# Kernel optimization log

Hardware: AMD Instinct MI355X
Metric: run time of the kernel (lower is better)

Reference implementation:

```python
import jax, jax.numpy as jnp
import numpy as np

B, S, D_MODEL, N_HEADS, D_FF = 4, 2048, 1024, 16, 4096
HEAD_DIM = D_MODEL // N_HEADS
NUM_BUCKETS, MAX_DISTANCE = 32, 128
EPS = 1e-6


def _relative_position_bucket(relative_position, num_buckets=NUM_BUCKETS, max_distance=MAX_DISTANCE):
    # bidirectional (encoder) variant, matching T5RelativePositionBias
    n = -relative_position
    nb = num_buckets // 2
    ret = (n < 0).astype(jnp.int32) * nb
    n = jnp.abs(n)
    max_exact = nb // 2
    val_if_large = max_exact + (
        jnp.log(jnp.maximum(n, 1).astype(jnp.float32) / max_exact)
        / np.log(max_distance / max_exact) * (nb - max_exact)
    ).astype(jnp.int32)
    val_if_large = jnp.minimum(val_if_large, nb - 1)
    return ret + jnp.where(n < max_exact, n, val_if_large)


def t5_position_bias(rel_emb, q_len, k_len):
    ctx = jnp.arange(q_len)[:, None]
    mem = jnp.arange(k_len)[None, :]
    rp_bucket = _relative_position_bucket(mem - ctx)          # [S, S]
    bias = rel_emb[rp_bucket]                                  # [S, S, H]
    return jnp.transpose(bias, (2, 0, 1))[None]                # [1, H, S, S]


def layer_norm(x, g, b):
    mu = jnp.mean(x, axis=-1, keepdims=True)
    var = jnp.mean(jnp.square(x - mu), axis=-1, keepdims=True)
    return (x - mu) * jax.lax.rsqrt(var + EPS) * g + b


def setup_inputs() -> dict:
    key = jax.random.key(0)
    ks = jax.random.split(key, 20)
    s = 0.02
    p = {
        'src': jax.random.normal(ks[0], (B, S, D_MODEL), jnp.float32),
        'wq': jax.random.normal(ks[1], (D_MODEL, D_MODEL), jnp.float32) * s,
        'bq': jnp.zeros((D_MODEL,), jnp.float32),
        'wk': jax.random.normal(ks[2], (D_MODEL, D_MODEL), jnp.float32) * s,
        'bk': jnp.zeros((D_MODEL,), jnp.float32),
        'wv': jax.random.normal(ks[3], (D_MODEL, D_MODEL), jnp.float32) * s,
        'bv': jnp.zeros((D_MODEL,), jnp.float32),
        'wo': jax.random.normal(ks[4], (D_MODEL, D_MODEL), jnp.float32) * s,
        'bo': jnp.zeros((D_MODEL,), jnp.float32),
        'w1': jax.random.normal(ks[5], (D_MODEL, D_FF), jnp.float32) * s,
        'b1': jnp.zeros((D_FF,), jnp.float32),
        'w2': jax.random.normal(ks[6], (D_FF, D_MODEL), jnp.float32) * s,
        'b2': jnp.zeros((D_MODEL,), jnp.float32),
        'ln1_g': jnp.ones((D_MODEL,), jnp.float32),
        'ln1_b': jnp.zeros((D_MODEL,), jnp.float32),
        'ln2_g': jnp.ones((D_MODEL,), jnp.float32),
        'ln2_b': jnp.zeros((D_MODEL,), jnp.float32),
        'rel_emb': jax.random.normal(ks[7], (NUM_BUCKETS, N_HEADS), jnp.float32) * s,
    }
    return p


def reference(src, wq, bq, wk, bk, wv, bv, wo, bo, w1, b1, w2, b2,
              ln1_g, ln1_b, ln2_g, ln2_b, rel_emb):
    b, s, _ = src.shape

    # --- self-attention block (pre-norm) ---
    xn = layer_norm(src, ln1_g, ln1_b)
    q = (xn @ wq + bq).reshape(b, s, N_HEADS, HEAD_DIM).transpose(0, 2, 1, 3)
    k = (xn @ wk + bk).reshape(b, s, N_HEADS, HEAD_DIM).transpose(0, 2, 1, 3)
    v = (xn @ wv + bv).reshape(b, s, N_HEADS, HEAD_DIM).transpose(0, 2, 1, 3)

    bias = t5_position_bias(rel_emb, s, s)                       # [1,H,S,S]
    scores = jnp.einsum('bhqd,bhkd->bhqk', q, k) / np.sqrt(HEAD_DIM) + bias
    attn = jax.nn.softmax(scores, axis=-1)
    ctx = jnp.einsum('bhqk,bhkd->bhqd', attn, v)                 # [B,H,S,Dh]
    ctx = ctx.transpose(0, 2, 1, 3).reshape(b, s, D_MODEL)
    x = src + (ctx @ wo + bo)

    # --- FFN block (pre-norm, ReLU) ---
    yn = layer_norm(x, ln2_g, ln2_b)
    y = jax.nn.relu(yn @ w1 + b1) @ w2 + b2
    return x + y
```

## Files before the change

kernel.cpp:

```cpp
#include <hip/hip_runtime.h>
#include <math.h>

typedef unsigned short u16;

#define S_LEN 2048
#define BSZ 4
#define DM 1024
#define NH 16
#define HD 64
#define DFF 4096
#define ROWS (BSZ * S_LEN)
#define LOG2E 1.4426950408889634f

typedef __attribute__((__ext_vector_type__(8))) __bf16 bf16x8;
typedef __attribute__((__ext_vector_type__(8))) short short8;
typedef __attribute__((__ext_vector_type__(4))) short short4v;
typedef __attribute__((__ext_vector_type__(4))) float f32x4;
typedef __attribute__((__ext_vector_type__(4))) float float4v;

__device__ __forceinline__ float bf2f(u16 u) {
    union { unsigned int i; float f; } c; c.i = ((unsigned int)u) << 16; return c.f;
}
__device__ __forceinline__ u16 f2bf(float f) {
    union { float f; unsigned int i; } c; c.f = f;
    unsigned int r = c.i + 0x7fffu + ((c.i >> 16) & 1u);
    return (u16)(r >> 16);
}
__device__ __forceinline__ u16 f2bf_cvt(float f) {
    __bf16 h = (__bf16)f;
    return __builtin_bit_cast(u16, h);
}
__device__ __forceinline__ float ldin(const void* p, long i, int f32) {
    return f32 ? ((const float*)p)[i] : bf2f(((const u16*)p)[i]);
}
__device__ __forceinline__ int dtype_f32(const u16* ln1g) {
    return ln1g[0] != 0x3F80;
}
__device__ __forceinline__ void gl_lds16(const void* g, void* l) {
    __builtin_amdgcn_global_load_lds(
        (const __attribute__((address_space(1))) unsigned int*)g,
        (__attribute__((address_space(3))) unsigned int*)l, 16, 0, 0);
}

__device__ __forceinline__ void tr_tile(
    const void* __restrict__ src, u16* __restrict__ dst, int N, int K,
    int bx, int by, int f32, int tid, u16 (*t)[72])
{
#pragma unroll
    for (int i = 0; i < 2; i++) {
        int c = tid + i * 256;
        int row = c >> 3, col = (c & 7) * 8;
        long off = (long)(by * 64 + row) * N + bx * 64 + col;
        short8 v;
        if (f32) {
            const float* s = (const float*)src + off;
            float4v a = *(const float4v*)s;
            float4v b = *(const float4v*)(s + 4);
#pragma unroll
            for (int k = 0; k < 4; k++) { v[k] = (short)f2bf(a[k]); v[k + 4] = (short)f2bf(b[k]); }
        } else {
            v = *(const short8*)((const u16*)src + off);
        }
        *(short8*)(&t[row][col]) = v;
    }
    __syncthreads();
#pragma unroll
    for (int i = 0; i < 2; i++) {
        int c = tid + i * 256;
        int row = c >> 3, col = (c & 7) * 8;
        short8 v;
#pragma unroll
        for (int jj = 0; jj < 8; jj++) v[jj] = (short)t[col + jj][row];
        *(short8*)(dst + (long)(bx * 64 + row) * K + by * 64 + col) = v;
    }
}

__global__ __launch_bounds__(256) void transpose4(
    const void* wq, const void* wk, const void* wv, const void* wo,
    u16* __restrict__ wqkvt, u16* __restrict__ wot, const u16* __restrict__ ln1g)
{
    __shared__ u16 t[64][72];
    int z = blockIdx.z;
    const void* src = (z == 0) ? wq : (z == 1) ? wk : (z == 2) ? wv : wo;
    u16* dst = (z < 3) ? wqkvt + (long)z * 1024 * 1024 : wot;
    tr_tile(src, dst, DM, DM, blockIdx.x, blockIdx.y, dtype_f32(ln1g), threadIdx.x, t);
}

__global__ __launch_bounds__(256) void transpose2(
    const void* w1, const void* w2, u16* __restrict__ w1t, u16* __restrict__ w2t,
    const u16* __restrict__ ln1g)
{
    __shared__ u16 t[64][72];
    int f32 = dtype_f32(ln1g);
    if (blockIdx.z == 0)
        tr_tile(w1, w1t, DFF, DM, blockIdx.x, blockIdx.y, f32, threadIdx.x, t);
    else
        tr_tile(w2, w2t, DM, DFF, blockIdx.y, blockIdx.x, f32, threadIdx.x, t);
}

__global__ __launch_bounds__(256) void vtrans(
    const u16* __restrict__ v, u16* __restrict__ vt)
{
    __shared__ u16 t[64][72];
    int s0 = blockIdx.x * 64;
    int bh = blockIdx.y;
    const u16* src = v + (long)bh * S_LEN * HD;
    u16* dst = vt + (long)bh * HD * S_LEN;
    int tid = threadIdx.x;
#pragma unroll
    for (int i = 0; i < 2; i++) {
        int c = tid + i * 256;
        int row = c >> 3, col = (c & 7) * 8;
        *(short8*)(&t[row][col]) = *(const short8*)(src + (long)(s0 + row) * HD + col);
    }
    __syncthreads();
#pragma unroll
    for (int i = 0; i < 2; i++) {
        int c = tid + i * 256;
        int row = c >> 3, col = (c & 7) * 8;
        short8 o;
#pragma unroll
        for (int jj = 0; jj < 8; jj++) o[jj] = (short)t[col + jj][row];
        *(short8*)(dst + (long)row * S_LEN + s0 + col) = o;
    }
}

__global__ __launch_bounds__(256) void prep_kernel(
    const void* bq, const void* bk, const void* bv, const void* bo,
    const void* b1, const void* b2, const void* l1g, const void* l1b,
    const void* l2g, const void* l2b, const void* rel,
    u16* __restrict__ smalls, float* __restrict__ bias_full)
{
    int f32 = dtype_f32((const u16*)l1g);
    int tid = blockIdx.x * blockDim.x + threadIdx.x;
    if (tid < 13312) {
        float v;
        if      (tid < 1024)  v = ldin(bq,  tid,         f32);
        else if (tid < 2048)  v = ldin(bk,  tid - 1024,  f32);
        else if (tid < 3072)  v = ldin(bv,  tid - 2048,  f32);
        else if (tid < 4096)  v = ldin(bo,  tid - 3072,  f32);
        else if (tid < 8192)  v = ldin(b1,  tid - 4096,  f32);
        else if (tid < 9216)  v = ldin(b2,  tid - 8192,  f32);
        else if (tid < 10240) v = ldin(l1g, tid - 9216,  f32);
        else if (tid < 11264) v = ldin(l1b, tid - 10240, f32);
        else if (tid < 12288) v = ldin(l2g, tid - 11264, f32);
        else                  v = ldin(l2b, tid - 12288, f32);
        smalls[tid] = f2bf(v);
    }
    if (tid < 4095 * 16) {
        int dIdx = tid >> 4;
        int h = tid & 15;
        int delta = dIdx - 2047;
        int n = -delta;
        int ret = (n < 0) ? 16 : 0;
        int na = (n < 0) ? -n : n;
        int bkt;
        if (na < 8) {
            bkt = na;
        } else {
            float tval = logf((float)na * 0.125f) * 2.8853900817779268f;
            int v = 8 + (int)tval;
            bkt = v < 15 ? v : 15;
        }
        bkt += ret;
        bias_full[h * 4095 + dIdx] = ldin(rel, bkt * 16 + h, f32) * LOG2E;
    }
}

__global__ __launch_bounds__(256) void ln_kernel(
    const void* __restrict__ xin, int external, const u16* __restrict__ ln1g,
    const u16* __restrict__ g, const u16* __restrict__ bta, u16* __restrict__ out)
{
    int f32 = external ? dtype_f32(ln1g) : 0;
    int row = blockIdx.x;
    int tid = threadIdx.x;
    float vals[4];
    if (f32) {
        float4v v = *(const float4v*)((const float*)xin + (long)row * DM + tid * 4);
#pragma unroll
        for (int k = 0; k < 4; k++) vals[k] = v[k];
    } else {
        short4v v = *(const short4v*)((const u16*)xin + (long)row * DM + tid * 4);
#pragma unroll
        for (int k = 0; k < 4; k++) vals[k] = bf2f((u16)v[k]);
    }
    float s1 = 0.f, s2 = 0.f;
#pragma unroll
    for (int k = 0; k < 4; k++) { s1 += vals[k]; s2 += vals[k] * vals[k]; }
#pragma unroll
    for (int off = 32; off > 0; off >>= 1) {
        s1 += __shfl_xor(s1, off);
        s2 += __shfl_xor(s2, off);
    }
    __shared__ float ps1[4], ps2[4];
    int wave = tid >> 6, lane = tid & 63;
    if (lane == 0) { ps1[wave] = s1; ps2[wave] = s2; }
    __syncthreads();
    s1 = ps1[0] + ps1[1] + ps1[2] + ps1[3];
    s2 = ps2[0] + ps2[1] + ps2[2] + ps2[3];
    float mu = s1 * (1.0f / DM);
    float var = s2 * (1.0f / DM) - mu * mu;
    float rs = rsqrtf(var + 1e-6f);
    short4v ov;
#pragma unroll
    for (int k = 0; k < 4; k++) {
        float gv = bf2f(g[tid * 4 + k]);
        float bv = bf2f(bta[tid * 4 + k]);
        ov[k] = (short)f2bf((vals[k] - mu) * rs * gv + bv);
    }
    *(short4v*)(out + (long)row * DM + tid * 4) = ov;
}

#define BM 128
#define BN 128
#define BK 64

__global__ __launch_bounds__(256, 3) void gemm_bt(
    const u16* __restrict__ A, const u16* __restrict__ Bt,
    const u16* __restrict__ bias, int M, int N, int K, int mode,
    u16* __restrict__ out_q, u16* __restrict__ out_k, u16* __restrict__ out_v,
    const void* __restrict__ res, void* __restrict__ outp,
    const u16* __restrict__ ln1g)
{
    __shared__ u16 As[BM][BK];
    __shared__ u16 Bs[BN][BK];
    int tid = threadIdx.x;
    int wave = tid >> 6, lane = tid & 63;
    int quad = lane >> 4, l16 = lane & 15;
    int wr = (wave >> 1) * 64, wc = (wave & 1) * 64;

    int nwg = gridDim.x * gridDim.y;
    int bid = blockIdx.y * gridDim.x + blockIdx.x;
    int chunk = nwg >> 3;
    int swz = (bid & 7) * chunk + (bid >> 3);
    int bx = swz % gridDim.x, by = swz / gridDim.x;

    long m0 = (long)by * BM, n0 = (long)bx * BN;
    int flg = (mode == 2 || mode == 4) ? dtype_f32(ln1g) : 0;

    int prow = tid >> 3;
    int pchk = tid & 7;
    int cchk = pchk ^ (prow & 7);
    int skc = cchk * 8;
    int pkc = pchk * 8;
    int rxor = l16 & 7;

    f32x4 acc[4][4];
    f32x4 z = {0.f, 0.f, 0.f, 0.f};
#pragma unroll
    for (int i = 0; i < 4; i++)
#pragma unroll
        for (int j = 0; j < 4; j++) acc[i][j] = z;

    for (int k0 = 0; k0 < K; k0 += BK) {
        __syncthreads();
#pragma unroll
        for (int ro = 0; ro < 4; ro++) {
            gl_lds16(A  + (m0 + ro * 32 + prow) * K + k0 + skc, &As[ro * 32 + prow][pkc]);
            gl_lds16(Bt + (n0 + ro * 32 + prow) * K + k0 + skc, &Bs[ro * 32 + prow][pkc]);
        }
        __syncthreads();
#pragma unroll
        for (int t = 0; t < 2; t++) {
            int rc = ((t * 4 + quad) ^ rxor) * 8;
            bf16x8 af[4], bfr[4];
#pragma unroll
            for (int i = 0; i < 4; i++)
                af[i] = __builtin_bit_cast(bf16x8, *(const short8*)(&As[wr + i * 16 + l16][rc]));
#pragma unroll
            for (int j = 0; j < 4; j++)
                bfr[j] = __builtin_bit_cast(bf16x8, *(const short8*)(&Bs[wc + j * 16 + l16][rc]));
#pragma unroll
            for (int i = 0; i < 4; i++)
#pragma unroll
                for (int j = 0; j < 4; j++)
                    acc[i][j] = __builtin_amdgcn_mfma_f32_16x16x32_bf16(af[i], bfr[j], acc[i][j], 0, 0, 0);
        }
    }

#pragma unroll
    for (int i = 0; i < 4; i++) {
#pragma unroll
        for (int j = 0; j < 4; j++) {
#pragma unroll
            for (int r = 0; r < 4; r++) {
                long gr = m0 + wr + i * 16 + quad * 4 + r;
                long gc = n0 + wc + j * 16 + l16;
                float val = acc[i][j][r] + bf2f(bias[gc]);
                if (mode == 1) {
                    int sel = (int)(gc >> 10);
                    int cc = (int)(gc & 1023);
                    int h = cc >> 6, d = cc & 63;
                    int b = (int)(gr >> 11), s = (int)(gr & 2047);
                    u16* dst = (sel == 0) ? out_q : (sel == 1 ? out_k : out_v);
                    dst[(((long)(b * NH + h)) * S_LEN + s) * HD + d] = f2bf(val);
                } else if (mode == 2) {
                    long idx = gr * N + gc;
                    float rv = flg ? ((const float*)res)[idx]
                                   : bf2f(((const u16*)res)[idx]);
                    ((u16*)outp)[idx] = f2bf(val + rv);
                } else if (mode == 3) {
                    ((u16*)outp)[gr * N + gc] = f2bf(val > 0.f ? val : 0.f);
                } else {
                    long idx = gr * N + gc;
                    float o = val + bf2f(((const u16*)res)[idx]);
                    if (flg) ((float*)outp)[idx] = o;
                    else     ((u16*)outp)[idx]  = f2bf(o);
                }
            }
        }
    }
}

__global__ __launch_bounds__(256, 4) void attn_kernel(
    const u16* __restrict__ Qg, const u16* __restrict__ Kg, const u16* __restrict__ Vtg,
    const float* __restrict__ bias_full, u16* __restrict__ ctx)
{
    __shared__ u16 Ks[64][64];
    __shared__ u16 Vt[64][64];
    __shared__ u16 Ps[64][72];
    __shared__ u16 bias_s[2112];

    int bh = blockIdx.y;
    int b = bh >> 4, h = bh & 15;
    int q0 = blockIdx.x * 64;
    const u16* Q  = Qg  + (long)bh * S_LEN * HD;
    const u16* Kp = Kg  + (long)bh * S_LEN * HD;
    const u16* Vp = Vtg + (long)bh * HD * S_LEN;

    int tid = threadIdx.x;
    int wave = tid >> 6, lane = tid & 63;
    int quad = lane >> 4, l16 = lane & 15;

    for (int i = tid; i < 2112; i += 256)
        bias_s[i] = f2bf(bias_full[h * 4095 + 1984 + i - q0]);
    float Bneg = bias_full[h * 4095 + 0];
    float Bpos = bias_full[h * 4095 + 4094];

    int prow = tid >> 3, pchk = tid & 7;
    int cchk = pchk ^ (prow & 7);
    int rxor = l16 & 7;
    int rc0 = (quad ^ rxor) * 8;
    int rc1 = ((4 + quad) ^ rxor) * 8;

    bf16x8 aq[2];
#pragma unroll
    for (int t = 0; t < 2; t++)
        aq[t] = __builtin_bit_cast(bf16x8,
            *(const short8*)(Q + (long)(q0 + wave * 16 + l16) * HD + t * 32 + quad * 8));

    bf16x8 ones;
#pragma unroll
    for (int i = 0; i < 8; i++) ones[i] = (__bf16)1.0f;

    f32x4 o[4];
    f32x4 z = {0.f, 0.f, 0.f, 0.f};
#pragma unroll
    for (int j = 0; j < 4; j++) o[j] = z;
    f32x4 lacc = z;

    int ib = 63 + quad * 4 - wave * 16 - l16;
    const float c0 = 0.125f * LOG2E;

    for (int t0 = 0; t0 < S_LEN; t0 += 64) {
        __syncthreads();
#pragma unroll
        for (int ro = 0; ro < 2; ro++) {
            gl_lds16(Kp + (long)(t0 + ro * 32 + prow) * HD + cchk * 8,
                     &Ks[ro * 32 + prow][pchk * 8]);
            gl_lds16(Vp + (long)(ro * 32 + prow) * S_LEN + t0 + cchk * 8,
                     &Vt[ro * 32 + prow][pchk * 8]);
        }
        __syncthreads();

        f32x4 s_[4];
#pragma unroll
        for (int j = 0; j < 4; j++) {
            f32x4 a = z;
            bf16x8 kf0 = __builtin_bit_cast(bf16x8, *(const short8*)(&Ks[j * 16 + l16][rc0]));
            a = __builtin_amdgcn_mfma_f32_16x16x32_bf16(kf0, aq[0], a, 0, 0, 0);
            bf16x8 kf1 = __builtin_bit_cast(bf16x8, *(const short8*)(&Ks[j * 16 + l16][rc1]));
            a = __builtin_amdgcn_mfma_f32_16x16x32_bf16(kf1, aq[1], a, 0, 0, 0);
            s_[j] = a;
        }
        int d0 = t0 - q0;
        int nearb = (d0 >= -153 && d0 <= 153);
        float bconst = (d0 > 0) ? Bpos : Bneg;
#pragma unroll
        for (int j = 0; j < 4; j++) {
            short4v pk;
#pragma unroll
            for (int r = 0; r < 4; r++) {
                float bl = nearb ? bf2f(bias_s[ib + t0 + j * 16 + r]) : bconst;
                float p = __builtin_amdgcn_exp2f(fminf(fmaf(s_[j][r], c0, bl), 100.0f));
                pk[r] = (short)f2bf_cvt(p);
            }
            *(short4v*)(&Ps[wave * 16 + l16][j * 16 + quad * 4]) = pk;
        }

        bf16x8 ap[2];
#pragma unroll
        for (int tt = 0; tt < 2; tt++)
            ap[tt] = __builtin_bit_cast(bf16x8,
                *(const short8*)(&Ps[wave * 16 + l16][tt * 32 + quad * 8]));
        lacc = __builtin_amdgcn_mfma_f32_16x16x32_bf16(ap[0], ones, lacc, 0, 0, 0);
        lacc = __builtin_amdgcn_mfma_f32_16x16x32_bf16(ap[1], ones, lacc, 0, 0, 0);
#pragma unroll
        for (int j = 0; j < 4; j++) {
            f32x4 t = o[j];
            bf16x8 bv0 = __builtin_bit_cast(bf16x8, *(const short8*)(&Vt[j * 16 + l16][rc0]));
            t = __builtin_amdgcn_mfma_f32_16x16x32_bf16(ap[0], bv0, t, 0, 0, 0);
            bf16x8 bv1 = __builtin_bit_cast(bf16x8, *(const short8*)(&Vt[j * 16 + l16][rc1]));
            t = __builtin_amdgcn_mfma_f32_16x16x32_bf16(ap[1], bv1, t, 0, 0, 0);
            o[j] = t;
        }
    }

#pragma unroll
    for (int r = 0; r < 4; r++) {
        int qr = wave * 16 + quad * 4 + r;
        float linv = 1.0f / lacc[r];
        long srow = (long)(b * S_LEN + q0 + qr);
#pragma unroll
        for (int j = 0; j < 4; j++)
            ctx[srow * DM + h * HD + j * 16 + l16] = f2bf(o[j][r] * linv);
    }
}

extern "C" void kernel_launch(void* const* d_in, const int* in_sizes, int n_in,
                              void* d_out, int out_size, void* d_ws, size_t ws_size,
                              hipStream_t stream)
{
    const void* src  = d_in[0];
    const void* wq   = d_in[1];
    const void* bq   = d_in[2];
    const void* wk   = d_in[3];
    const void* bk   = d_in[4];
    const void* wv   = d_in[5];
    const void* bv   = d_in[6];
    const void* wo   = d_in[7];
    const void* bo   = d_in[8];
    const void* w1   = d_in[9];
    const void* b1   = d_in[10];
    const void* w2   = d_in[11];
    const void* b2   = d_in[12];
    const void* ln1g = d_in[13];
    const void* ln1b = d_in[14];
    const void* ln2g = d_in[15];
    const void* ln2b = d_in[16];
    const void* rel  = d_in[17];
    const u16* l1g16 = (const u16*)ln1g;

    char* ws = (char*)d_ws;
    const long MB = 1L << 20;
    u16*   smalls = (u16*)  (ws);
    float* bfull  = (float*)(ws + 65536);
    u16*   xn     = (u16*)  (ws + 1  * MB);
    u16*   vtg    = (u16*)  (ws + 1  * MB);
    u16*   qws    = (u16*)  (ws + 17 * MB);
    u16*   kws    = (u16*)  (ws + 33 * MB);
    u16*   vws    = (u16*)  (ws + 49 * MB);
    u16*   hbuf   = (u16*)  (ws + 1  * MB);
    u16*   ctx    = (u16*)  (ws + 65 * MB);
    u16*   yn     = (u16*)  (ws + 65 * MB);
    u16*   xbf    = (u16*)  (ws + 81 * MB);
    u16*   wqkvt  = (u16*)  (ws + 97 * MB);
    u16*   wot    = (u16*)  (ws + 103 * MB);
    u16*   w1t    = (u16*)  (ws + 97 * MB);
    u16*   w2t    = (u16*)  (ws + 105 * MB);

    transpose4<<<dim3(16, 16, 4), 256, 0, stream>>>(wq, wk, wv, wo, wqkvt, wot, l1g16);
    prep_kernel<<<256, 256, 0, stream>>>(bq, bk, bv, bo, b1, b2,
                                         ln1g, ln1b, ln2g, ln2b, rel,
                                         smalls, bfull);

    ln_kernel<<<ROWS, 256, 0, stream>>>(src, 1, l1g16,
                                        smalls + 9216, smalls + 10240, xn);

    gemm_bt<<<dim3(3072 / BN, ROWS / BM), 256, 0, stream>>>(
        xn, wqkvt, smalls + 0, ROWS, 3072, DM, 1,
        qws, kws, vws, nullptr, nullptr, l1g16);

    vtrans<<<dim3(S_LEN / 64, BSZ * NH), 256, 0, stream>>>(vws, vtg);

    attn_kernel<<<dim3(S_LEN / 64, BSZ * NH), 256, 0, stream>>>(qws, kws, vtg, bfull, ctx);

    gemm_bt<<<dim3(DM / BN, ROWS / BM), 256, 0, stream>>>(
        ctx, wot, smalls + 3072, ROWS, DM, DM, 2,
        nullptr, nullptr, nullptr, src, xbf, l1g16);

    transpose2<<<dim3(64, 16, 2), 256, 0, stream>>>(w1, w2, w1t, w2t, l1g16);

    ln_kernel<<<ROWS, 256, 0, stream>>>(xbf, 0, l1g16,
                                        smalls + 11264, smalls + 12288, yn);

    gemm_bt<<<dim3(DFF / BN, ROWS / BM), 256, 0, stream>>>(
        yn, w1t, smalls + 4096, ROWS, DFF, DM, 3,
        nullptr, nullptr, nullptr, nullptr, hbuf, l1g16);

    gemm_bt<<<dim3(DM / BN, ROWS / BM), 256, 0, stream>>>(
        hbuf, w2t, smalls + 8192, ROWS, DM, DFF, 4,
        nullptr, nullptr, nullptr, xbf, d_out, l1g16);
}
```

Measured before the change: 597.4 us.

## Add 256x256 pipelined GEMM kernel for QKV and FFN1 projections

Introduces a new 512-thread GEMM with 256x256 output tiles, double-buffered LDS fed by direct global-to-LDS loads, XOR-swizzled LDS layout, and a hand-scheduled phase pipeline using explicit waitcnt/barrier and setprio. Workgroup IDs are remapped so neighbouring blocks share operands in cache. The QKV and FFN-up projections switch to this kernel to raise arithmetic intensity per LDS load and overlap memory with MFMA. The larger tiles produce fewer workgroups (e.g. 384 for QKV), which may underfill the GPU, and the manual vmcnt accounting is fragile.

```diff
diff --git a/kernel.cpp b/kernel.cpp
--- a/kernel.cpp
+++ b/kernel.cpp
@@ -41,6 +41,11 @@
         (const __attribute__((address_space(1))) unsigned int*)g,
         (__attribute__((address_space(3))) unsigned int*)l, 16, 0, 0);
 }
+
+#define BARR  asm volatile("s_barrier" ::: "memory")
+#define LGKM0 asm volatile("s_waitcnt lgkmcnt(0)" ::: "memory")
+#define VM4   asm volatile("s_waitcnt vmcnt(4)" ::: "memory")
+#define VM0   asm volatile("s_waitcnt vmcnt(0)" ::: "memory")
 
 __device__ __forceinline__ void tr_tile(
     const void* __restrict__ src, u16* __restrict__ dst, int N, int K,
@@ -312,6 +317,145 @@
     }
 }
 
+#define TM 256
+#define TN 256
+#define TK 64
+
+#define PHASE(bi, q, STAGE, WAITV)                                             \
+    {                                                                          \
+        if ((q) == 0) {                                                        \
+            _Pragma("unroll")                                                  \
+            for (int j = 0; j < 4; j++) {                                      \
+                _Pragma("unroll")                                              \
+                for (int t = 0; t < 2; t++)                                    \
+                    bfr[j][t] = __builtin_bit_cast(bf16x8, *(const short8*)(   \
+                        &Bs[bi][wn * 64 + j * 16 + l16][((t * 4 + quad) ^ rxor) * 8])); \
+            }                                                                  \
+        }                                                                      \
+        _Pragma("unroll")                                                      \
+        for (int i = 0; i < 2; i++) {                                          \
+            _Pragma("unroll")                                                  \
+            for (int t = 0; t < 2; t++)                                        \
+                af[i][t] = __builtin_bit_cast(bf16x8, *(const short8*)(        \
+                    &As[bi][wm * 128 + ((q) * 2 + i) * 16 + l16][((t * 4 + quad) ^ rxor) * 8])); \
+        }                                                                      \
+        STAGE                                                                  \
+        WAITV;                                                                 \
+        BARR;                                                                  \
+        LGKM0;                                                                 \
+        __builtin_amdgcn_sched_barrier(0);                                     \
+        __builtin_amdgcn_s_setprio(1);                                         \
+        _Pragma("unroll")                                                      \
+        for (int i = 0; i < 2; i++) {                                          \
+            _Pragma("unroll")                                                  \
+            for (int j = 0; j < 4; j++) {                                      \
+                acc[(q) * 2 + i][j] = __builtin_amdgcn_mfma_f32_16x16x32_bf16( \
+                    af[i][0], bfr[j][0], acc[(q) * 2 + i][j], 0, 0, 0);        \
+                acc[(q) * 2 + i][j] = __builtin_amdgcn_mfma_f32_16x16x32_bf16( \
+                    af[i][1], bfr[j][1], acc[(q) * 2 + i][j], 0, 0, 0);        \
+            }                                                                  \
+        }                                                                      \
+        __builtin_amdgcn_s_setprio(0);                                         \
+        BARR;                                                                  \
+    }
+
+__global__ __launch_bounds__(512, 2) void gemm256(
+    const u16* __restrict__ A, const u16* __restrict__ Bt,
+    const u16* __restrict__ bias, int M, int N, int K, int mode,
+    u16* __restrict__ out_q, u16* __restrict__ out_k, u16* __restrict__ out_v,
+    u16* __restrict__ outp)
+{
+    __shared__ u16 As[2][TM][TK];
+    __shared__ u16 Bs[2][TN][TK];
+
+    int tid = threadIdx.x;
+    int wavei = tid >> 6, lane = tid & 63;
+    int quad = lane >> 4, l16 = lane & 15;
+    int wm = wavei >> 2, wn = wavei & 3;
+
+    int nwg = gridDim.x * gridDim.y;
+    int bid = blockIdx.y * gridDim.x + blockIdx.x;
+    int chunk = nwg >> 3;
+    int swz = (bid & 7) * chunk + (bid >> 3);
+    int bx = swz % gridDim.x, by = swz / gridDim.x;
+    long m0 = (long)by * TM, n0 = (long)bx * TN;
+
+    int srow = tid >> 3;
+    int pchk = tid & 7;
+    int cchk = pchk ^ (srow & 7);
+    int rxor = l16 & 7;
+
+    int NT = K / TK;
+
+    auto stageA = [&](int bufi, int h, int t) {
+        const u16* g = A + (m0 + h * 128 + srow) * (long)K + (long)t * TK + cchk * 8;
+        gl_lds16(g,                 &As[bufi][h * 128 + srow     ][pchk * 8]);
+        gl_lds16(g + 64 * (long)K,  &As[bufi][h * 128 + srow + 64][pchk * 8]);
+    };
+    auto stageB = [&](int bufi, int h, int t) {
+        const u16* g = Bt + (n0 + h * 128 + srow) * (long)K + (long)t * TK + cchk * 8;
+        gl_lds16(g,                 &Bs[bufi][h * 128 + srow     ][pchk * 8]);
+        gl_lds16(g + 64 * (long)K,  &Bs[bufi][h * 128 + srow + 64][pchk * 8]);
+    };
+
+    f32x4 acc[8][4];
+    f32x4 z = {0.f, 0.f, 0.f, 0.f};
+#pragma unroll
+    for (int i = 0; i < 8; i++)
+#pragma unroll
+        for (int j = 0; j < 4; j++) acc[i][j] = z;
+
+    bf16x8 bfr[4][2];
+    bf16x8 af[2][2];
+
+    stageA(0, 0, 0); stageA(0, 1, 0); stageB(0, 0, 0); stageB(0, 1, 0);
+    stageB(1, 0, 1); stageB(1, 1, 1);
+    VM4;
+    BARR;
+
+    for (int kt = 0; kt < NT - 2; kt += 2) {
+        PHASE(0, 0, { stageA(1, 0, kt + 1); stageA(1, 1, kt + 1); }, (void)0);
+        PHASE(0, 1, { stageB(0, 0, kt + 2); }, (void)0);
+        PHASE(0, 2, { stageB(0, 1, kt + 2); }, (void)0);
+        PHASE(0, 3, {}, VM4);
+        PHASE(1, 0, { stageA(0, 0, kt + 2); }, (void)0);
+        PHASE(1, 1, { stageA(0, 1, kt + 2); stageB(1, 0, kt + 3); }, (void)0);
+        PHASE(1, 2, { stageB(1, 1, kt + 3); }, (void)0);
+        PHASE(1, 3, {}, VM4);
+    }
+    PHASE(0, 0, { stageA(1, 0, NT - 1); stageA(1, 1, NT - 1); }, (void)0);
+    PHASE(0, 1, {}, (void)0);
+    PHASE(0, 2, {}, (void)0);
+    PHASE(0, 3, {}, VM0);
+    PHASE(1, 0, {}, (void)0);
+    PHASE(1, 1, {}, (void)0);
+    PHASE(1, 2, {}, (void)0);
+    PHASE(1, 3, {}, (void)0);
+
+#pragma unroll
+    for (int i = 0; i < 8; i++) {
+#pragma unroll
+        for (int j = 0; j < 4; j++) {
+#pragma unroll
+            for (int r = 0; r < 4; r++) {
+                long gr = m0 + wm * 128 + i * 16 + quad * 4 + r;
+                long gc = n0 + wn * 64 + j * 16 + l16;
+                float val = acc[i][j][r] + bf2f(bias[gc]);
+                if (mode == 1) {
+                    int sel = (int)(gc >> 10);
+                    int cc = (int)(gc & 1023);
+                    int h = cc >> 6, d = cc & 63;
+                    int b = (int)(gr >> 11), s = (int)(gr & 2047);
+                    u16* dst = (sel == 0) ? out_q : (sel == 1 ? out_k : out_v);
+                    dst[(((long)(b * NH + h)) * S_LEN + s) * HD + d] = f2bf(val);
+                } else {
+                    outp[gr * (long)N + gc] = f2bf(val > 0.f ? val : 0.f);
+                }
+            }
+        }
+    }
+}
+
 __global__ __launch_bounds__(256, 4) void attn_kernel(
     const u16* __restrict__ Qg, const u16* __restrict__ Kg, const u16* __restrict__ Vtg,
     const float* __restrict__ bias_full, u16* __restrict__ ctx)
@@ -477,9 +621,8 @@
     ln_kernel<<<ROWS, 256, 0, stream>>>(src, 1, l1g16,
                                         smalls + 9216, smalls + 10240, xn);
 
-    gemm_bt<<<dim3(3072 / BN, ROWS / BM), 256, 0, stream>>>(
-        xn, wqkvt, smalls + 0, ROWS, 3072, DM, 1,
-        qws, kws, vws, nullptr, nullptr, l1g16);
+    gemm256<<<dim3(3072 / TN, ROWS / TM), 512, 0, stream>>>(
+        xn, wqkvt, smalls + 0, ROWS, 3072, DM, 1, qws, kws, vws, nullptr);
 
     vtrans<<<dim3(S_LEN / 64, BSZ * NH), 256, 0, stream>>>(vws, vtg);
 
@@ -494,9 +637,8 @@
     ln_kernel<<<ROWS, 256, 0, stream>>>(xbf, 0, l1g16,
                                         smalls + 11264, smalls + 12288, yn);
 
-    gemm_bt<<<dim3(DFF / BN, ROWS / BM), 256, 0, stream>>>(
-        yn, w1t, smalls + 4096, ROWS, DFF, DM, 3,
-        nullptr, nullptr, nullptr, nullptr, hbuf, l1g16);
+    gemm256<<<dim3(DFF / TN, ROWS / TM), 512, 0, stream>>>(
+        yn, w1t, smalls + 4096, ROWS, DFF, DM, 3, nullptr, nullptr, nullptr, hbuf);
 
     gemm_bt<<<dim3(DM / BN, ROWS / BM), 256, 0, stream>>>(
         hbuf, w2t, smalls + 8192, ROWS, DM, DFF, 4,
```

Result: no change. 586.3 us (-1.9%).
